# Performance work log

Measured on AMD Instinct MI355X. Metric: run time of the kernel, lower is better.

Reference implementation:

```python
import jax, jax.numpy as jnp
import numpy as np

D_MODEL = 256; H = 8; D_FF = 1024; BLOCKS = 2
NUM_ITEMS = 200000; NUM_USERS = 100000; T_DLT = 512
B = 256; INTER = 50; INTRA = 20; CAND = 2048
NEG_INF = -1e9

def layer_norm(x, g, b, eps=1e-6):
    m = x.mean(-1, keepdims=True)
    s = x.std(-1, keepdims=True, ddof=1)  # torch .std is unbiased
    return g * (x - m) / (s + eps) + b

def pos_encoding(L, d):
    pos = jnp.arange(L, dtype=jnp.float32)[:, None]
    div = jnp.exp(jnp.arange(0, d, 2, dtype=jnp.float32) * (-jnp.log(10000.0) / d))
    pe = jnp.zeros((L, d), dtype=jnp.float32)
    pe = pe.at[:, 0::2].set(jnp.sin(pos * div))
    pe = pe.at[:, 1::2].set(jnp.cos(pos * div))
    return pe

def setup_inputs() -> dict:
    key = jax.random.key(0)
    ks = jax.random.split(key, 20)
    d = D_MODEL
    w = lambda k, shape, s: jax.random.normal(k, shape, dtype=jnp.float32) * s
    s = 1.0 / np.sqrt(d)
    inp = {}
    inp["item_emb"] = w(ks[0], (NUM_ITEMS, d), 0.02)
    inp["user_emb"] = w(ks[1], (NUM_USERS, d), 0.02)
    inp["time_emb"] = w(ks[2], (T_DLT, d), 0.02)
    inp["Wq"] = w(ks[3], (d, d), s); inp["bq"] = jnp.zeros((d,), jnp.float32)
    inp["Wk"] = w(ks[4], (d, d), s); inp["bk"] = jnp.zeros((d,), jnp.float32)
    inp["Wv"] = w(ks[5], (d, d), s); inp["bv"] = jnp.zeros((d,), jnp.float32)
    inp["Wo"] = w(ks[6], (d, d), s); inp["bo"] = jnp.zeros((d,), jnp.float32)
    inp["ln1_g"] = jnp.ones((d,), jnp.float32); inp["ln1_b"] = jnp.zeros((d,), jnp.float32)
    inp["W1"] = w(ks[7], (d, D_FF), s); inp["b1"] = jnp.zeros((D_FF,), jnp.float32)
    inp["W2"] = w(ks[8], (D_FF, d), 1.0 / np.sqrt(D_FF)); inp["b2"] = jnp.zeros((d,), jnp.float32)
    inp["ln2_g"] = jnp.ones((d,), jnp.float32); inp["ln2_b"] = jnp.zeros((d,), jnp.float32)
    inp["fn_g"] = jnp.ones((d,), jnp.float32); inp["fn_b"] = jnp.zeros((d,), jnp.float32)
    inp["gate_Wl"] = w(ks[9], (d, d), s)
    inp["gate_Ws"] = w(ks[10], (d, d), s)
    inp["gate_Wt"] = w(ks[11], (d, d), s)
    inp["gate_bias"] = w(ks[12], (1, d), s)
    inp["batch_us"] = jax.random.randint(ks[13], (B,), 1, NUM_USERS)
    inp["batch_sessions"] = jax.random.randint(ks[14], (B, INTER, INTRA), 0, NUM_ITEMS)
    inp["batch_timedlt"] = jax.random.randint(ks[15], (B,), 0, T_DLT)
    inp["batch_to_predict"] = jax.random.randint(ks[16], (B, CAND), 1, NUM_ITEMS)
    return inp

def reference(item_emb, user_emb, time_emb, Wq, bq, Wk, bk, Wv, bv, Wo, bo,
              ln1_g, ln1_b, W1, b1, W2, b2, ln2_g, ln2_b, fn_g, fn_b,
              gate_Wl, gate_Ws, gate_Wt, gate_bias,
              batch_us, batch_sessions, batch_timedlt, batch_to_predict):
    d = D_MODEL
    item_e = item_emb.at[0].set(0.0)  # padding_idx=0
    user_e = user_emb.at[0].set(0.0)
    E = item_e[batch_sessions]              # [B, INTER, INTRA, d]
    U_embs = user_e[batch_us]               # [B, d]
    t_embs = time_emb[batch_timedlt]        # [B, d]
    Bsz = E.shape[0]
    # intra-session attention (single-head scaled dot-product, padding mask only)
    x = E.reshape(-1, INTRA, d)             # [B*INTER, INTRA, d]
    pad1 = (batch_sessions.reshape(-1, INTRA) != 0)[:, None, :]
    scores = jnp.einsum('nqd,nkd->nqk', x, x) / jnp.sqrt(jnp.float32(d))
    p = jax.nn.softmax(jnp.where(pad1, scores, NEG_INF), axis=-1)
    atted = jnp.einsum('nqk,nkd->nqd', p, x)
    E_hat = atted.sum(axis=1).reshape(Bsz, INTER, d)
    u_short = E_hat[:, -1, :]
    pad2 = (batch_sessions[:, :, 0] != 0)[:, None, None, :]   # [B,1,1,INTER]
    S = E_hat + pos_encoding(INTER, d)[None]
    dh = d // H
    for _ in range(BLOCKS):  # same sublayer applied blocks times (shared weights)
        y = layer_norm(S, ln1_g, ln1_b)
        q = (y @ Wq + bq).reshape(Bsz, INTER, H, dh)
        k = (y @ Wk + bk).reshape(Bsz, INTER, H, dh)
        v = (y @ Wv + bv).reshape(Bsz, INTER, H, dh)
        att = jnp.einsum('bqhe,bkhe->bhqk', q, k) / jnp.sqrt(jnp.float32(dh))
        aw = jax.nn.softmax(jnp.where(pad2, att, NEG_INF), axis=-1)
        o = jnp.einsum('bhqk,bkhe->bqhe', aw, v).reshape(Bsz, INTER, d)
        S = S + o @ Wo + bo
        y2 = layer_norm(S, ln2_g, ln2_b)
        S = S + jax.nn.relu(y2 @ W1 + b1) @ W2 + b2
    S1 = layer_norm(S, fn_g, fn_b)
    u_long = S1.sum(axis=1) + U_embs
    Tg = jax.nn.sigmoid(u_long @ gate_Wl + u_short @ gate_Ws + t_embs @ gate_Wt + gate_bias)
    U = Tg * u_short + (1.0 - Tg) * u_long
    cand = item_e[batch_to_predict]         # [B, CAND, d]
    return jnp.einsum('bcd,bd->bc', cand, U)
```

## Files before the change

### kernel.cpp

```cpp
#include <hip/hip_runtime.h>
#include <math.h>

#define D 256
#define HEADS 8
#define DH 32
#define INTER 50
#define INTRA 20
#define BSZ 256
#define CANDN 2048
#define ROWS (BSZ*INTER)
#define NITEMS 200000

typedef unsigned short ushort_t;
typedef __attribute__((ext_vector_type(8))) short bf16x8;
typedef __attribute__((ext_vector_type(4))) float f32x4;

__device__ __forceinline__ unsigned short f2b(float f) {
    union { float f; unsigned u; } v; v.f = f;
    unsigned r = v.u + 0x7fffu + ((v.u >> 16) & 1u);
    return (unsigned short)(r >> 16);
}
__device__ __forceinline__ float b2f(unsigned short h) {
    union { unsigned u; float f; } v; v.u = ((unsigned)h) << 16;
    return v.f;
}

__device__ __forceinline__ void wtr_body(const float* __restrict__ W, int K, int N,
    unsigned short* __restrict__ WT, int bx, int by, float (*tile)[33], int t)
{
    int n0 = bx*32, k0 = by*32;
    int tx = t & 31, ty = t >> 5;
    for (int i = ty; i < 32; i += 8)
        tile[i][tx] = W[(size_t)(k0+i)*N + n0 + tx];
    __syncthreads();
    for (int i = ty; i < 32; i += 8)
        WT[(size_t)(n0+i)*K + k0 + tx] = f2b(tile[tx][i]);
}

__global__ __launch_bounds__(256) void prep_k(
    const float* __restrict__ item_emb, unsigned short* __restrict__ item_b, int itemBlocks,
    const float* __restrict__ Wq, const float* __restrict__ Wk,
    const float* __restrict__ Wv, const float* __restrict__ Wo,
    const float* __restrict__ W1, const float* __restrict__ W2,
    unsigned short* __restrict__ WqkvT, unsigned short* __restrict__ WoT,
    unsigned short* __restrict__ W1T, unsigned short* __restrict__ W2T,
    const float* __restrict__ bq, const float* __restrict__ bk,
    const float* __restrict__ bv, float* __restrict__ bqkv)
{
    __shared__ float tile[32][33];
    int blk = blockIdx.x, t = threadIdx.x;
    if (blk < itemBlocks) {
        int i = blk*256 + t;
        float4 v = ((const float4*)item_emb)[i];
        ushort4 h; h.x=f2b(v.x); h.y=f2b(v.y); h.z=f2b(v.z); h.w=f2b(v.w);
        ((ushort4*)item_b)[i] = h;
        return;
    }
    blk -= itemBlocks;
    if (blk < 64)       wtr_body(Wq, 256, 256,  WqkvT,            blk & 7,  blk >> 3, tile, t);
    else if (blk < 128) wtr_body(Wk, 256, 256,  WqkvT + 256*256, (blk-64) & 7,  (blk-64) >> 3, tile, t);
    else if (blk < 192) wtr_body(Wv, 256, 256,  WqkvT + 512*256, (blk-128) & 7, (blk-128) >> 3, tile, t);
    else if (blk < 256) wtr_body(Wo, 256, 256,  WoT,             (blk-192) & 7, (blk-192) >> 3, tile, t);
    else if (blk < 512) { int id = blk-256; wtr_body(W1, 256, 1024, W1T, id & 31, id >> 5, tile, t); }
    else if (blk < 768) { int id = blk-512; wtr_body(W2, 1024, 256, W2T, id & 7,  id >> 3, tile, t); }
    else { bqkv[t] = bq[t]; bqkv[256+t] = bk[t]; bqkv[512+t] = bv[t]; }
}

#define XST 264
__global__ __launch_bounds__(256) void intra_k(
    const float* __restrict__ item_emb, const unsigned short* __restrict__ item_b,
    const int* __restrict__ sess,
    float* __restrict__ S, float* __restrict__ u_short)
{
    __shared__ __align__(16) unsigned short xb[4][INTRA][XST];
    __shared__ __align__(16) unsigned short zrow[XST];
    __shared__ float sc[4][20][21];
    __shared__ float wsum[4][20];
    __shared__ int ids[4][INTRA];
    int t = threadIdx.x, w = t >> 6, lane = t & 63;
    int s = blockIdx.x*4 + w;
    if (lane < INTRA) ids[w][lane] = sess[s*INTRA + lane];
    if (t < 132) ((unsigned int*)zrow)[t] = 0u;
    __syncthreads();
    int col = lane*4;
    for (int r = 0; r < INTRA; ++r) {
        int id = ids[w][r];
        ushort4 h;
        if (id == 0) { h.x=h.y=h.z=h.w=0; }
        else if (item_b) {
            h = *(const ushort4*)(item_b + (size_t)id*D + col);
        } else {
            float4 v4 = *(const float4*)(item_emb + (size_t)id*D + col);
            h.x=f2b(v4.x); h.y=f2b(v4.y); h.z=f2b(v4.z); h.w=f2b(v4.w);
        }
        *(ushort4*)&xb[w][r][col] = h;
    }
    __syncthreads();
    int ml = lane & 15, q8 = (lane >> 4) * 8;
    int r1 = 16 + ml;
    f32x4 acc[2][2] = {};
    for (int k0 = 0; k0 < D; k0 += 32) {
        bf16x8 fr0 = *(const bf16x8*)&xb[w][ml][k0 + q8];
        bf16x8 fr1 = (r1 < INTRA) ? *(const bf16x8*)&xb[w][r1][k0 + q8]
                                  : *(const bf16x8*)&zrow[q8];
        acc[0][0] = __builtin_amdgcn_mfma_f32_16x16x32_bf16(fr0, fr0, acc[0][0], 0,0,0);
        acc[0][1] = __builtin_amdgcn_mfma_f32_16x16x32_bf16(fr0, fr1, acc[0][1], 0,0,0);
        acc[1][0] = __builtin_amdgcn_mfma_f32_16x16x32_bf16(fr1, fr0, acc[1][0], 0,0,0);
        acc[1][1] = __builtin_amdgcn_mfma_f32_16x16x32_bf16(fr1, fr1, acc[1][1], 0,0,0);
    }
    int rb = (lane >> 4) * 4;
    #pragma unroll
    for (int mt = 0; mt < 2; ++mt)
        #pragma unroll
        for (int nt = 0; nt < 2; ++nt)
            #pragma unroll
            for (int i = 0; i < 4; ++i) {
                int row = mt*16 + rb + i, cc = nt*16 + ml;
                if (row < INTRA && cc < INTRA) sc[w][row][cc] = acc[mt][nt][i];
            }
    __syncthreads();
    if (lane < INTRA) {
        float vrow[INTRA]; float mx = -1e30f;
        #pragma unroll
        for (int k = 0; k < INTRA; ++k) {
            float v_ = (ids[w][k] != 0) ? sc[w][lane][k]*(1.0f/16.0f) : -1e9f;
            vrow[k] = v_; mx = fmaxf(mx, v_);
        }
        float ssum = 0.f;
        #pragma unroll
        for (int k = 0; k < INTRA; ++k) { float e_ = expf(vrow[k]-mx); vrow[k]=e_; ssum+=e_; }
        float inv = 1.f/ssum;
        #pragma unroll
        for (int k = 0; k < INTRA; ++k) sc[w][lane][k] = vrow[k]*inv;
    }
    __syncthreads();
    if (lane < INTRA) {
        float s_ = 0.f;
        #pragma unroll
        for (int q = 0; q < INTRA; ++q) s_ += sc[w][q][lane];
        wsum[w][lane] = s_;
    }
    __syncthreads();
    float4 v = {0.f,0.f,0.f,0.f};
    #pragma unroll
    for (int k = 0; k < INTRA; ++k) {
        float ws_ = wsum[w][k];
        ushort4 h = *(const ushort4*)&xb[w][k][col];
        v.x += ws_*b2f(h.x); v.y += ws_*b2f(h.y);
        v.z += ws_*b2f(h.z); v.w += ws_*b2f(h.w);
    }
    int b = s / INTER, srow = s % INTER;
    if (srow == INTER-1) *(float4*)(u_short + (size_t)b*D + col) = v;
    const float kc = -9.210340371976184f / 256.0f;
    float div0 = expf((float)col * kc);
    float div2 = expf((float)(col+2) * kc);
    float4 o;
    o.x = v.x + sinf((float)srow * div0);
    o.y = v.y + cosf((float)srow * div0);
    o.z = v.z + sinf((float)srow * div2);
    o.w = v.w + cosf((float)srow * div2);
    *(float4*)(S + (size_t)s*D + col) = o;
}

#define LB_VT 0
#define LB_Y 36864
#define LB_Q 70656
#define LB_K 104448
#define LB_PB 36864
#define LB_O 110592
#define LB_SL 0
#define LB_Y2 52000
#define LB_H 85792
#define LB_MSK 152352
#define MFMA16(a,b,c) __builtin_amdgcn_mfma_f32_16x16x32_bf16(a, b, c, 0, 0, 0)

__global__ __launch_bounds__(512) void block_k(
    float* __restrict__ S,
    const unsigned short* __restrict__ WqkvT, const float* __restrict__ bqkv,
    const unsigned short* __restrict__ WoT, const float* __restrict__ bo,
    const unsigned short* __restrict__ W1T, const float* __restrict__ b1,
    const unsigned short* __restrict__ W2T, const float* __restrict__ b2,
    const float* __restrict__ ln1_g, const float* __restrict__ ln1_b,
    const float* __restrict__ ln2_g, const float* __restrict__ ln2_b,
    const int* __restrict__ sess)
{
    __shared__ __align__(16) char LB[152608];
    unsigned short* Yp  = (unsigned short*)(LB + LB_Y);
    unsigned short* Qp  = (unsigned short*)(LB + LB_Q);
    unsigned short* Kp  = (unsigned short*)(LB + LB_K);
    unsigned short* VTp = (unsigned short*)(LB + LB_VT);
    unsigned short* Op  = (unsigned short*)(LB + LB_O);
    unsigned short* Y2p = (unsigned short*)(LB + LB_Y2);
    unsigned short* Hp  = (unsigned short*)(LB + LB_H);
    float* Slp  = (float*)(LB + LB_SL);
    float* mskp = (float*)(LB + LB_MSK);

    int b = blockIdx.x;
    int t = threadIdx.x, w = t >> 6, lane = t & 63;
    int ml = lane & 15, q8 = (lane >> 4) * 8;
    int col_l = ml, rbase = (lane >> 4) * 4;
    float* Sg = S + (size_t)b * INTER * D;

    if (t < 64) mskp[t] = (t < 50 && sess[(b*INTER + t)*INTRA] != 0) ? 1.f : 0.f;
    for (int u = t; u < 14*256; u += 512) {
        int r = 50 + (u >> 8), c = u & 255;
        Yp[r*264 + c] = 0; Qp[r*264 + c] = 0; Kp[r*264 + c] = 0;
    }
    for (int u = t; u < 8*32*14; u += 512) {
        int hh = u / 448, rem = u % 448;
        VTp[(hh*32 + rem/14)*72 + 50 + rem%14] = 0;
    }
    {
        int col = lane*4;
        float4 g4 = *(const float4*)(ln1_g + col), b4 = *(const float4*)(ln1_b + col);
        for (int r = w; r < 50; r += 8) {
            float4 x = *(const float4*)(Sg + r*256 + col);
            float s_ = x.x + x.y + x.z + x.w;
            #pragma unroll
            for (int o = 32; o > 0; o >>= 1) s_ += __shfl_xor(s_, o, 64);
            float mean = s_ * (1.f/256.f);
            float dx = x.x-mean, dy = x.y-mean, dz = x.z-mean, dw = x.w-mean;
            float qq = dx*dx + dy*dy + dz*dz + dw*dw;
            #pragma unroll
            for (int o = 32; o > 0; o >>= 1) qq += __shfl_xor(qq, o, 64);
            float inv = 1.f/(sqrtf(qq*(1.f/255.f)) + 1e-6f);
            ushort4 h;
            h.x = f2b(g4.x*dx*inv + b4.x); h.y = f2b(g4.y*dy*inv + b4.y);
            h.z = f2b(g4.z*dz*inv + b4.z); h.w = f2b(g4.w*dw*inv + b4.w);
            *(ushort4*)&Yp[r*264 + col] = h;
        }
    }
    __syncthreads();

    {
        f32x4 acc[4][6] = {};
        #pragma unroll
        for (int ks = 0; ks < 8; ++ks) {
            bf16x8 af[4];
            #pragma unroll
            for (int mt = 0; mt < 4; ++mt)
                af[mt] = *(const bf16x8*)&Yp[(mt*16+ml)*264 + ks*32 + q8];
            bf16x8 bfr[6];
            #pragma unroll
            for (int j = 0; j < 6; ++j) {
                int n = (w*6 + j)*16 + ml;
                bfr[j] = *(const bf16x8*)(WqkvT + (size_t)n*256 + ks*32 + q8);
            }
            #pragma unroll
            for (int j = 0; j < 6; ++j)
                #pragma unroll
                for (int mt = 0; mt < 4; ++mt)
                    acc[mt][j] = MFMA16(af[mt], bfr[j], acc[mt][j]);
        }
        #pragma unroll
        for (int j = 0; j < 6; ++j) {
            int n = (w*6 + j)*16 + col_l;
            float bs = bqkv[n];
            #pragma unroll
            for (int mt = 0; mt < 4; ++mt)
                #pragma unroll
                for (int i = 0; i < 4; ++i) {
                    int row = mt*16 + rbase + i;
                    if (row < 50) {
                        unsigned short hv = f2b(acc[mt][j][i] + bs);
                        if (n < 256)      Qp[row*264 + n] = hv;
                        else if (n < 512) Kp[row*264 + (n-256)] = hv;
                        else { int hh=(n-512)>>5, e=(n-512)&31; VTp[(hh*32+e)*72 + row] = hv; }
                    }
                }
        }
    }
    __syncthreads();

    unsigned short* pbw = (unsigned short*)(LB + LB_PB + w*9216);
    {
        f32x4 p3[4][4] = {};
        {
            bf16x8 af[4], bf_[4];
            #pragma unroll
            for (int mt = 0; mt < 4; ++mt)
                af[mt] = *(const bf16x8*)&Qp[(mt*16+ml)*264 + w*32 + q8];
            #pragma unroll
            for (int nt = 0; nt < 4; ++nt)
                bf_[nt] = *(const bf16x8*)&Kp[(nt*16+ml)*264 + w*32 + q8];
            #pragma unroll
            for (int mt = 0; mt < 4; ++mt)
                #pragma unroll
                for (int nt = 0; nt < 4; ++nt)
                    p3[mt][nt] = MFMA16(af[mt], bf_[nt], p3[mt][nt]);
        }
        float mk[4];
        #pragma unroll
        for (int nt = 0; nt < 4; ++nt) mk[nt] = mskp[nt*16 + ml];
        __syncthreads();
        #pragma unroll
        for (int mt = 0; mt < 4; ++mt)
            #pragma unroll
            for (int i = 0; i < 4; ++i) {
                int row = mt*16 + rbase + i;
                float v[4]; float m = -1e30f;
                #pragma unroll
                for (int nt = 0; nt < 4; ++nt) {
                    float x = (mk[nt] != 0.f) ? p3[mt][nt][i]*0.17677669529663687f : -1e9f;
                    v[nt] = x; m = fmaxf(m, x);
                }
                #pragma unroll
                for (int o = 8; o > 0; o >>= 1) m = fmaxf(m, __shfl_xor(m, o, 64));
                float s_ = 0.f;
                #pragma unroll
                for (int nt = 0; nt < 4; ++nt) { v[nt] = expf(v[nt] - m); s_ += v[nt]; }
                #pragma unroll
                for (int o = 8; o > 0; o >>= 1) s_ += __shfl_xor(s_, o, 64);
                float inv = 1.f / s_;
                if (row < 50) {
                    #pragma unroll
                    for (int nt = 0; nt < 4; ++nt)
                        pbw[row*72 + nt*16 + ml] = f2b(v[nt]*inv);
                }
            }
    }
    {
        f32x4 po[4][2] = {};
        #pragma unroll
        for (int kt = 0; kt < 2; ++kt) {
            bf16x8 af[4], bv_[2];
            #pragma unroll
            for (int mt = 0; mt < 4; ++mt)
                af[mt] = *(const bf16x8*)&pbw[(mt*16+ml)*72 + kt*32 + q8];
            #pragma unroll
            for (int nt = 0; nt < 2; ++nt)
                bv_[nt] = *(const bf16x8*)&VTp[(w*32 + nt*16 + ml)*72 + kt*32 + q8];
            #pragma unroll
            for (int nt = 0; nt < 2; ++nt)
                #pragma unroll
                for (int mt = 0; mt < 4; ++mt)
                    po[mt][nt] = MFMA16(af[mt], bv_[nt], po[mt][nt]);
        }
        #pragma unroll
        for (int nt = 0; nt < 2; ++nt)
            #pragma unroll
            for (int mt = 0; mt < 4; ++mt)
                #pragma unroll
                for (int i = 0; i < 4; ++i) {
                    int row = mt*16 + rbase + i;
                    if (row < 50)
                        Op[row*264 + w*32 + nt*16 + col_l] = f2b(po[mt][nt][i]);
                }
    }
    __syncthreads();

    {
        f32x4 a5[4][2] = {};
        #pragma unroll
        for (int ks = 0; ks < 8; ++ks) {
            bf16x8 af[4], bw[2];
            #pragma unroll
            for (int mt = 0; mt < 4; ++mt)
                af[mt] = *(const bf16x8*)&Op[(mt*16+ml)*264 + ks*32 + q8];
            #pragma unroll
            for (int j = 0; j < 2; ++j) {
                int n = w*32 + j*16 + ml;
                bw[j] = *(const bf16x8*)(WoT + (size_t)n*256 + ks*32 + q8);
            }
            #pragma unroll
            for (int j = 0; j < 2; ++j)
                #pragma unroll
                for (int mt = 0; mt < 4; ++mt)
                    a5[mt][j] = MFMA16(af[mt], bw[j], a5[mt][j]);
        }
        #pragma unroll
        for (int j = 0; j < 2; ++j) {
            int n = w*32 + j*16 + col_l;
            float bv = bo[n];
            #pragma unroll
            for (int mt = 0; mt < 4; ++mt)
                #pragma unroll
                for (int i = 0; i < 4; ++i) {
                    int row = mt*16 + rbase + i;
                    if (row < 50)
                        Slp[row*260 + n] = Sg[row*256 + n] + a5[mt][j][i] + bv;
                }
        }
    }
    __syncthreads();

    {
        int col = lane*4;
        float4 g4 = *(const float4*)(ln2_g + col), b4 = *(const float4*)(ln2_b + col);
        for (int r = w; r < 50; r += 8) {
            float4 x = *(const float4*)&Slp[r*260 + col];
            float s_ = x.x + x.y + x.z + x.w;
            #pragma unroll
            for (int o = 32; o > 0; o >>= 1) s_ += __shfl_xor(s_, o, 64);
            float mean = s_ * (1.f/256.f);
            float dx = x.x-mean, dy = x.y-mean, dz = x.z-mean, dw = x.w-mean;
            float qq = dx*dx + dy*dy + dz*dz + dw*dw;
            #pragma unroll
            for (int o = 32; o > 0; o >>= 1) qq += __shfl_xor(qq, o, 64);
            float inv = 1.f/(sqrtf(qq*(1.f/255.f)) + 1e-6f);
            ushort4 h;
            h.x = f2b(g4.x*dx*inv + b4.x); h.y = f2b(g4.y*dy*inv + b4.y);
            h.z = f2b(g4.z*dz*inv + b4.z); h.w = f2b(g4.w*dw*inv + b4.w);
            *(ushort4*)&Y2p[r*264 + col] = h;
        }
        for (int u = t; u < 14*256; u += 512) {
            int r = 50 + (u >> 8), c = u & 255;
            Y2p[r*264 + c] = 0;
        }
    }
    __syncthreads();

    #pragma unroll
    for (int hf = 0; hf < 2; ++hf) {
        {
            f32x4 a7[4][4] = {};
            #pragma unroll
            for (int ks = 0; ks < 8; ++ks) {
                bf16x8 af[4], bw[4];
                #pragma unroll
                for (int mt = 0; mt < 4; ++mt)
                    af[mt] = *(const bf16x8*)&Y2p[(mt*16+ml)*264 + ks*32 + q8];
                #pragma unroll
                for (int j = 0; j < 4; ++j) {
                    int n = hf*512 + w*64 + j*16 + ml;
                    bw[j] = *(const bf16x8*)(W1T + (size_t)n*256 + ks*32 + q8);
                }
                #pragma unroll
                for (int j = 0; j < 4; ++j)
                    #pragma unroll
                    for (int mt = 0; mt < 4; ++mt)
                        a7[mt][j] = MFMA16(af[mt], bw[j], a7[mt][j]);
            }
            #pragma unroll
            for (int j = 0; j < 4; ++j) {
                int nl = w*64 + j*16 + col_l;
                float bv = b1[hf*512 + nl];
                #pragma unroll
                for (int mt = 0; mt < 4; ++mt)
                    #pragma unroll
                    for (int i = 0; i < 4; ++i) {
                        int row = mt*16 + rbase + i;
                        if (row < 50)
                            Hp[row*520 + nl] = f2b(fmaxf(a7[mt][j][i] + bv, 0.f));
                    }
            }
        }
        __syncthreads();
        {
            f32x4 a8[4][2] = {};
            #pragma unroll
            for (int ks = 0; ks < 16; ++ks) {
                bf16x8 af[4], bw[2];
                #pragma unroll
                for (int mt = 0; mt < 4; ++mt)
                    af[mt] = *(const bf16x8*)&Hp[(mt*16+ml)*520 + ks*32 + q8];
                #pragma unroll
                for (int j = 0; j < 2; ++j) {
                    int n = w*32 + j*16 + ml;
                    bw[j] = *(const bf16x8*)(W2T + (size_t)n*1024 + hf*512 + ks*32 + q8);
                }
                #pragma unroll
                for (int j = 0; j < 2; ++j)
                    #pragma unroll
                    for (int mt = 0; mt < 4; ++mt)
                        a8[mt][j] = MFMA16(af[mt], bw[j], a8[mt][j]);
            }
            #pragma unroll
            for (int j = 0; j < 2; ++j) {
                int n = w*32 + j*16 + col_l;
                float bv = (hf == 0) ? b2[n] : 0.f;
                #pragma unroll
                for (int mt = 0; mt < 4; ++mt)
                    #pragma unroll
                    for (int i = 0; i < 4; ++i) {
                        int row = mt*16 + rbase + i;
                        if (row < 50)
                            Slp[row*260 + n] += a8[mt][j][i] + bv;
                    }
            }
        }
        __syncthreads();
    }

    for (int u = t; u < 50*256; u += 512) {
        int r = u >> 8, c = u & 255;
        Sg[r*256 + c] = Slp[r*260 + c];
    }
}

__global__ __launch_bounds__(256) void tail_k(
    const float* __restrict__ S,
    const float* __restrict__ fn_g, const float* __restrict__ fn_b,
    const float* __restrict__ user_emb, const int* __restrict__ us,
    const float* __restrict__ time_emb, const int* __restrict__ tdlt,
    const float* __restrict__ u_short,
    const float* __restrict__ Wl, const float* __restrict__ Ws,
    const float* __restrict__ Wt, const float* __restrict__ gb,
    float* __restrict__ U)
{
    __shared__ float part[4][D];
    __shared__ float ul[D], ush[D], te[D];
    int b = blockIdx.x, t = threadIdx.x, w = t >> 6, lane = t & 63;
    int col = lane*4;
    float4 g4 = *(const float4*)(fn_g + col);
    float4 b4 = *(const float4*)(fn_b + col);
    float4 acc4 = {0.f,0.f,0.f,0.f};
    for (int l = w; l < INTER; l += 4) {
        float4 x = *(const float4*)(S + (size_t)(b*INTER + l)*D + col);
        float s = x.x + x.y + x.z + x.w;
        #pragma unroll
        for (int o = 32; o > 0; o >>= 1) s += __shfl_xor(s, o, 64);
        float mean = s * (1.f/256.f);
        float dx = x.x - mean, dy = x.y - mean, dz = x.z - mean, dw = x.w - mean;
        float q = dx*dx + dy*dy + dz*dz + dw*dw;
        #pragma unroll
        for (int o = 32; o > 0; o >>= 1) q += __shfl_xor(q, o, 64);
        float inv = 1.f/(sqrtf(q*(1.f/255.f)) + 1e-6f);
        acc4.x += g4.x*dx*inv + b4.x;
        acc4.y += g4.y*dy*inv + b4.y;
        acc4.z += g4.z*dz*inv + b4.z;
        acc4.w += g4.w*dw*inv + b4.w;
    }
    *(float4*)&part[w][col] = acc4;
    __syncthreads();
    int id = us[b];
    float ue = (id == 0) ? 0.f : user_emb[(size_t)id*D + t];
    float ulv = part[0][t] + part[1][t] + part[2][t] + part[3][t] + ue;
    ul[t]  = ulv;
    float ushv = u_short[b*D + t];
    ush[t] = ushv;
    te[t]  = time_emb[(size_t)tdlt[b]*D + t];
    __syncthreads();
    float a = gb[t];
    for (int k = 0; k < D; ++k)
        a += ul[k]*Wl[k*D + t] + ush[k]*Ws[k*D + t] + te[k]*Wt[k*D + t];
    float tg = 1.f/(1.f + expf(-a));
    U[b*D + t] = tg*ushv + (1.f - tg)*ulv;
}

__global__ __launch_bounds__(256) void out_k(
    const float* __restrict__ item_emb, const unsigned short* __restrict__ item_b,
    const int* __restrict__ pred,
    const float* __restrict__ U, float* __restrict__ out)
{
    int b = blockIdx.x >> 6;
    int cbase = (blockIdx.x & 63) * 32;
    int t = threadIdx.x, w = t >> 6, lane = t & 63;
    int hl = lane & 31, half = lane >> 5;
    float4 u0 = *(const float4*)(U + (size_t)b*D + hl*8);
    float4 u1 = *(const float4*)(U + (size_t)b*D + hl*8 + 4);
    for (int it = 0; it < 4; ++it) {
        int c = cbase + it*8 + w*2 + half;
        int id = pred[b*CANDN + c];
        float p = 0.f;
        if (id) {
            if (item_b) {
                const unsigned short* row = item_b + (size_t)id*D + hl*8;
                ushort4 a = *(const ushort4*)row;
                ushort4 d = *(const ushort4*)(row+4);
                p = b2f(a.x)*u0.x + b2f(a.y)*u0.y + b2f(a.z)*u0.z + b2f(a.w)*u0.w
                  + b2f(d.x)*u1.x + b2f(d.y)*u1.y + b2f(d.z)*u1.z + b2f(d.w)*u1.w;
            } else {
                const float* row = item_emb + (size_t)id*D + hl*8;
                float4 a = *(const float4*)row;
                float4 d = *(const float4*)(row+4);
                p = a.x*u0.x + a.y*u0.y + a.z*u0.z + a.w*u0.w
                  + d.x*u1.x + d.y*u1.y + d.z*u1.z + d.w*u1.w;
            }
        }
        #pragma unroll
        for (int off = 16; off > 0; off >>= 1) p += __shfl_xor(p, off, 64);
        if (hl == 0) out[b*CANDN + c] = p;
    }
}

extern "C" void kernel_launch(void* const* d_in, const int* in_sizes, int n_in,
                              void* d_out, int out_size, void* d_ws, size_t ws_size,
                              hipStream_t stream)
{
    const float* item_emb = (const float*)d_in[0];
    const float* user_emb = (const float*)d_in[1];
    const float* time_emb = (const float*)d_in[2];
    const float* Wq = (const float*)d_in[3];  const float* bq = (const float*)d_in[4];
    const float* Wk = (const float*)d_in[5];  const float* bk = (const float*)d_in[6];
    const float* Wv = (const float*)d_in[7];  const float* bv = (const float*)d_in[8];
    const float* Wo = (const float*)d_in[9];  const float* bo = (const float*)d_in[10];
    const float* ln1_g = (const float*)d_in[11]; const float* ln1_b = (const float*)d_in[12];
    const float* W1 = (const float*)d_in[13]; const float* b1 = (const float*)d_in[14];
    const float* W2 = (const float*)d_in[15]; const float* b2 = (const float*)d_in[16];
    const float* ln2_g = (const float*)d_in[17]; const float* ln2_b = (const float*)d_in[18];
    const float* fn_g = (const float*)d_in[19]; const float* fn_b = (const float*)d_in[20];
    const float* gWl = (const float*)d_in[21]; const float* gWs = (const float*)d_in[22];
    const float* gWt = (const float*)d_in[23]; const float* gbias = (const float*)d_in[24];
    const int* us   = (const int*)d_in[25];
    const int* sess = (const int*)d_in[26];
    const int* tdlt = (const int*)d_in[27];
    const int* pred = (const int*)d_in[28];
    float* out = (float*)d_out;

    char* base = (char*)d_ws;
    size_t off = 0;
    float* S = (float*)(base+off);              off += (size_t)ROWS*D*4;
    unsigned short* WqkvT = (unsigned short*)(base+off); off += (size_t)768*256*2;
    unsigned short* WoT   = (unsigned short*)(base+off); off += (size_t)256*256*2;
    unsigned short* W1T   = (unsigned short*)(base+off); off += (size_t)1024*256*2;
    unsigned short* W2T   = (unsigned short*)(base+off); off += (size_t)256*1024*2;
    float* bqkv = (float*)(base+off);            off += 768*4;
    float* u_short = (float*)(base+off);         off += BSZ*D*4;
    float* Ufin    = (float*)(base+off);         off += BSZ*D*4;
    unsigned short* item_b = (unsigned short*)(base+off);
    size_t item_b_bytes = (size_t)NITEMS*D*2;
    bool use_b16 = (off + item_b_bytes) <= ws_size;
    if (!use_b16) item_b = nullptr;

    int itemBlocks = use_b16 ? (NITEMS*D/4)/256 : 0;
    prep_k<<<itemBlocks + 769, 256, 0, stream>>>(
        item_emb, item_b, itemBlocks,
        Wq, Wk, Wv, Wo, W1, W2,
        WqkvT, WoT, W1T, W2T,
        bq, bk, bv, bqkv);

    intra_k<<<ROWS/4, 256, 0, stream>>>(item_emb, item_b, sess, S, u_short);

    for (int blk = 0; blk < 2; ++blk)
        block_k<<<BSZ, 512, 0, stream>>>(S, WqkvT, bqkv, WoT, bo,
                                         W1T, b1, W2T, b2,
                                         ln1_g, ln1_b, ln2_g, ln2_b, sess);

    tail_k<<<BSZ, 256, 0, stream>>>(S, fn_g, fn_b, user_emb, us,
        time_emb, tdlt, u_short, gWl, gWs, gWt, gbias, Ufin);

    out_k<<<(BSZ*CANDN)/32, 256, 0, stream>>>(item_emb, item_b, pred, Ufin, out);
}
```

Baseline: 677.4 us.

## Fuse both transformer blocks and final norm into one 1024-thread kernel

Both shared-weight transformer blocks now run inside a single block_k launch that loops twice, so the second launch and part of the global reload of S go away. The final layer norm and the sum over the sequence move into the same kernel, which writes a per-batch u_long vector that tail_k reads. The workgroup grows from 512 to 1024 threads, and each wave takes half the earlier GEMM and attention work, meaning two waves per head. Zeroing of the padded Y, Q, K and Y2 rows is dropped; the code relies on masking and on discarding rows at or beyond 50 to keep results correct.

```diff
diff --git a/kernel.cpp b/kernel.cpp
--- a/kernel.cpp
+++ b/kernel.cpp
@@ -174,7 +174,7 @@
 #define LB_MSK 152352
 #define MFMA16(a,b,c) __builtin_amdgcn_mfma_f32_16x16x32_bf16(a, b, c, 0, 0, 0)
 
-__global__ __launch_bounds__(512) void block_k(
+__global__ __launch_bounds__(1024) void block_k(
     float* __restrict__ S,
     const unsigned short* __restrict__ WqkvT, const float* __restrict__ bqkv,
     const unsigned short* __restrict__ WoT, const float* __restrict__ bo,
@@ -182,7 +182,8 @@
     const unsigned short* __restrict__ W2T, const float* __restrict__ b2,
     const float* __restrict__ ln1_g, const float* __restrict__ ln1_b,
     const float* __restrict__ ln2_g, const float* __restrict__ ln2_b,
-    const int* __restrict__ sess)
+    const float* __restrict__ fn_g, const float* __restrict__ fn_b,
+    const int* __restrict__ sess, float* __restrict__ u_long_raw)
 {
     __shared__ __align__(16) char LB[152608];
     unsigned short* Yp  = (unsigned short*)(LB + LB_Y);
@@ -199,22 +200,282 @@
     int t = threadIdx.x, w = t >> 6, lane = t & 63;
     int ml = lane & 15, q8 = (lane >> 4) * 8;
     int col_l = ml, rbase = (lane >> 4) * 4;
+    int h = w >> 1, half = w & 1;
     float* Sg = S + (size_t)b * INTER * D;
 
     if (t < 64) mskp[t] = (t < 50 && sess[(b*INTER + t)*INTRA] != 0) ? 1.f : 0.f;
-    for (int u = t; u < 14*256; u += 512) {
-        int r = 50 + (u >> 8), c = u & 255;
-        Yp[r*264 + c] = 0; Qp[r*264 + c] = 0; Kp[r*264 + c] = 0;
-    }
-    for (int u = t; u < 8*32*14; u += 512) {
-        int hh = u / 448, rem = u % 448;
-        VTp[(hh*32 + rem/14)*72 + 50 + rem%14] = 0;
-    }
+
+    for (int blk = 0; blk < 2; ++blk) {
+        for (int u = t; u < 8*32*14; u += 1024) {
+            int hh = u / 448, rem = u % 448;
+            VTp[(hh*32 + rem/14)*72 + 50 + rem%14] = 0;
+        }
+        {
+            int col = lane*4;
+            float4 g4 = *(const float4*)(ln1_g + col), b4 = *(const float4*)(ln1_b + col);
+            for (int r = w; r < 50; r += 16) {
+                float4 x = *(const float4*)(Sg + r*256 + col);
+                float s_ = x.x + x.y + x.z + x.w;
+                #pragma unroll
+                for (int o = 32; o > 0; o >>= 1) s_ += __shfl_xor(s_, o, 64);
+                float mean = s_ * (1.f/256.f);
+                float dx = x.x-mean, dy = x.y-mean, dz = x.z-mean, dw = x.w-mean;
+                float qq = dx*dx + dy*dy + dz*dz + dw*dw;
+                #pragma unroll
+                for (int o = 32; o > 0; o >>= 1) qq += __shfl_xor(qq, o, 64);
+                float inv = 1.f/(sqrtf(qq*(1.f/255.f)) + 1e-6f);
+                ushort4 hh4;
+                hh4.x = f2b(g4.x*dx*inv + b4.x); hh4.y = f2b(g4.y*dy*inv + b4.y);
+                hh4.z = f2b(g4.z*dz*inv + b4.z); hh4.w = f2b(g4.w*dw*inv + b4.w);
+                *(ushort4*)&Yp[r*264 + col] = hh4;
+            }
+        }
+        __syncthreads();
+
+        {
+            f32x4 acc[4][3] = {};
+            #pragma unroll
+            for (int ks = 0; ks < 8; ++ks) {
+                bf16x8 af[4];
+                #pragma unroll
+                for (int mt = 0; mt < 4; ++mt)
+                    af[mt] = *(const bf16x8*)&Yp[(mt*16+ml)*264 + ks*32 + q8];
+                bf16x8 bfr[3];
+                #pragma unroll
+                for (int j = 0; j < 3; ++j) {
+                    int n = (w*3 + j)*16 + ml;
+                    bfr[j] = *(const bf16x8*)(WqkvT + (size_t)n*256 + ks*32 + q8);
+                }
+                #pragma unroll
+                for (int j = 0; j < 3; ++j)
+                    #pragma unroll
+                    for (int mt = 0; mt < 4; ++mt)
+                        acc[mt][j] = MFMA16(af[mt], bfr[j], acc[mt][j]);
+            }
+            #pragma unroll
+            for (int j = 0; j < 3; ++j) {
+                int n = (w*3 + j)*16 + col_l;
+                float bs = bqkv[n];
+                #pragma unroll
+                for (int mt = 0; mt < 4; ++mt)
+                    #pragma unroll
+                    for (int i = 0; i < 4; ++i) {
+                        int row = mt*16 + rbase + i;
+                        if (row < 50) {
+                            unsigned short hv = f2b(acc[mt][j][i] + bs);
+                            if (n < 256)      Qp[row*264 + n] = hv;
+                            else if (n < 512) Kp[row*264 + (n-256)] = hv;
+                            else { int hh=(n-512)>>5, e=(n-512)&31; VTp[(hh*32+e)*72 + row] = hv; }
+                        }
+                    }
+            }
+        }
+        __syncthreads();
+
+        unsigned short* pbw = (unsigned short*)(LB + LB_PB + h*9216);
+        {
+            f32x4 p3[2][4] = {};
+            {
+                bf16x8 af[2], bf_[4];
+                #pragma unroll
+                for (int mt2 = 0; mt2 < 2; ++mt2)
+                    af[mt2] = *(const bf16x8*)&Qp[((half*2+mt2)*16+ml)*264 + h*32 + q8];
+                #pragma unroll
+                for (int nt = 0; nt < 4; ++nt)
+                    bf_[nt] = *(const bf16x8*)&Kp[(nt*16+ml)*264 + h*32 + q8];
+                #pragma unroll
+                for (int mt2 = 0; mt2 < 2; ++mt2)
+                    #pragma unroll
+                    for (int nt = 0; nt < 4; ++nt)
+                        p3[mt2][nt] = MFMA16(af[mt2], bf_[nt], p3[mt2][nt]);
+            }
+            float mk[4];
+            #pragma unroll
+            for (int nt = 0; nt < 4; ++nt) mk[nt] = mskp[nt*16 + ml];
+            __syncthreads();
+            #pragma unroll
+            for (int mt2 = 0; mt2 < 2; ++mt2)
+                #pragma unroll
+                for (int i = 0; i < 4; ++i) {
+                    int row = (half*2+mt2)*16 + rbase + i;
+                    float v[4]; float m = -1e30f;
+                    #pragma unroll
+                    for (int nt = 0; nt < 4; ++nt) {
+                        float x = (mk[nt] != 0.f) ? p3[mt2][nt][i]*0.17677669529663687f : -1e9f;
+                        v[nt] = x; m = fmaxf(m, x);
+                    }
+                    #pragma unroll
+                    for (int o = 8; o > 0; o >>= 1) m = fmaxf(m, __shfl_xor(m, o, 64));
+                    float s_ = 0.f;
+                    #pragma unroll
+                    for (int nt = 0; nt < 4; ++nt) { v[nt] = expf(v[nt] - m); s_ += v[nt]; }
+                    #pragma unroll
+                    for (int o = 8; o > 0; o >>= 1) s_ += __shfl_xor(s_, o, 64);
+                    float inv = 1.f / s_;
+                    if (row < 50) {
+                        #pragma unroll
+                        for (int nt = 0; nt < 4; ++nt)
+                            pbw[row*72 + nt*16 + ml] = f2b(v[nt]*inv);
+                    }
+                }
+        }
+        {
+            f32x4 po[2][2] = {};
+            #pragma unroll
+            for (int kt = 0; kt < 2; ++kt) {
+                bf16x8 af[2], bv_[2];
+                #pragma unroll
+                for (int mt2 = 0; mt2 < 2; ++mt2)
+                    af[mt2] = *(const bf16x8*)&pbw[((half*2+mt2)*16+ml)*72 + kt*32 + q8];
+                #pragma unroll
+                for (int nt = 0; nt < 2; ++nt)
+                    bv_[nt] = *(const bf16x8*)&VTp[(h*32 + nt*16 + ml)*72 + kt*32 + q8];
+                #pragma unroll
+                for (int nt = 0; nt < 2; ++nt)
+                    #pragma unroll
+                    for (int mt2 = 0; mt2 < 2; ++mt2)
+                        po[mt2][nt] = MFMA16(af[mt2], bv_[nt], po[mt2][nt]);
+            }
+            #pragma unroll
+            for (int nt = 0; nt < 2; ++nt)
+                #pragma unroll
+                for (int mt2 = 0; mt2 < 2; ++mt2)
+                    #pragma unroll
+                    for (int i = 0; i < 4; ++i) {
+                        int row = (half*2+mt2)*16 + rbase + i;
+                        if (row < 50)
+                            Op[row*264 + h*32 + nt*16 + col_l] = f2b(po[mt2][nt][i]);
+                    }
+        }
+        __syncthreads();
+
+        {
+            f32x4 a5[4] = {};
+            #pragma unroll
+            for (int ks = 0; ks < 8; ++ks) {
+                bf16x8 af[4], bw;
+                #pragma unroll
+                for (int mt = 0; mt < 4; ++mt)
+                    af[mt] = *(const bf16x8*)&Op[(mt*16+ml)*264 + ks*32 + q8];
+                bw = *(const bf16x8*)(WoT + (size_t)(w*16+ml)*256 + ks*32 + q8);
+                #pragma unroll
+                for (int mt = 0; mt < 4; ++mt)
+                    a5[mt] = MFMA16(af[mt], bw, a5[mt]);
+            }
+            int n = w*16 + col_l;
+            float bv = bo[n];
+            #pragma unroll
+            for (int mt = 0; mt < 4; ++mt)
+                #pragma unroll
+                for (int i = 0; i < 4; ++i) {
+                    int row = mt*16 + rbase + i;
+                    if (row < 50)
+                        Slp[row*260 + n] = Sg[row*256 + n] + a5[mt][i] + bv;
+                }
+        }
+        __syncthreads();
+
+        {
+            int col = lane*4;
+            float4 g4 = *(const float4*)(ln2_g + col), b4 = *(const float4*)(ln2_b + col);
+            for (int r = w; r < 50; r += 16) {
+                float4 x = *(const float4*)&Slp[r*260 + col];
+                float s_ = x.x + x.y + x.z + x.w;
+                #pragma unroll
+                for (int o = 32; o > 0; o >>= 1) s_ += __shfl_xor(s_, o, 64);
+                float mean = s_ * (1.f/256.f);
+                float dx = x.x-mean, dy = x.y-mean, dz = x.z-mean, dw = x.w-mean;
+                float qq = dx*dx + dy*dy + dz*dz + dw*dw;
+                #pragma unroll
+                for (int o = 32; o > 0; o >>= 1) qq += __shfl_xor(qq, o, 64);
+                float inv = 1.f/(sqrtf(qq*(1.f/255.f)) + 1e-6f);
+                ushort4 hh4;
+                hh4.x = f2b(g4.x*dx*inv + b4.x); hh4.y = f2b(g4.y*dy*inv + b4.y);
+                hh4.z = f2b(g4.z*dz*inv + b4.z); hh4.w = f2b(g4.w*dw*inv + b4.w);
+                *(ushort4*)&Y2p[r*264 + col] = hh4;
+            }
+        }
+        __syncthreads();
+
+        #pragma unroll
+        for (int hf = 0; hf < 2; ++hf) {
+            {
+                f32x4 a7[4][2] = {};
+                #pragma unroll
+                for (int ks = 0; ks < 8; ++ks) {
+                    bf16x8 af[4], bw[2];
+                    #pragma unroll
+                    for (int mt = 0; mt < 4; ++mt)
+                        af[mt] = *(const bf16x8*)&Y2p[(mt*16+ml)*264 + ks*32 + q8];
+                    #pragma unroll
+                    for (int j = 0; j < 2; ++j) {
+                        int n = hf*512 + (w*2+j)*16 + ml;
+                        bw[j] = *(const bf16x8*)(W1T + (size_t)n*256 + ks*32 + q8);
+                    }
+                    #pragma unroll
+                    for (int j = 0; j < 2; ++j)
+                        #pragma unroll
+                        for (int mt = 0; mt < 4; ++mt)
+                            a7[mt][j] = MFMA16(af[mt], bw[j], a7[mt][j]);
+                }
+                #pragma unroll
+                for (int j = 0; j < 2; ++j) {
+                    int nl = (w*2+j)*16 + col_l;
+                    float bv = b1[hf*512 + nl];
+                    #pragma unroll
+                    for (int mt = 0; mt < 4; ++mt)
+                        #pragma unroll
+                        for (int i = 0; i < 4; ++i) {
+                            int row = mt*16 + rbase + i;
+                            if (row < 50)
+                                Hp[row*520 + nl] = f2b(fmaxf(a7[mt][j][i] + bv, 0.f));
+                        }
+                }
+            }
+            __syncthreads();
+            {
+                f32x4 a8[4] = {};
+                #pragma unroll
+                for (int ks = 0; ks < 16; ++ks) {
+                    bf16x8 af[4], bw;
+                    #pragma unroll
+                    for (int mt = 0; mt < 4; ++mt)
+                        af[mt] = *(const bf16x8*)&Hp[(mt*16+ml)*520 + ks*32 + q8];
+                    bw = *(const bf16x8*)(W2T + (size_t)(w*16+ml)*1024 + hf*512 + ks*32 + q8);
+                    #pragma unroll
+                    for (int mt = 0; mt < 4; ++mt)
+                        a8[mt] = MFMA16(af[mt], bw, a8[mt]);
+                }
+                int n = w*16 + col_l;
+                float bv = (hf == 0) ? b2[n] : 0.f;
+                #pragma unroll
+                for (int mt = 0; mt < 4; ++mt)
+                    #pragma unroll
+                    for (int i = 0; i < 4; ++i) {
+                        int row = mt*16 + rbase + i;
+                        if (row < 50)
+                            Slp[row*260 + n] += a8[mt][i] + bv;
+                    }
+            }
+            __syncthreads();
+        }
+
+        if (blk == 0) {
+            for (int u = t; u < 50*256; u += 1024) {
+                int r = u >> 8, c = u & 255;
+                Sg[r*256 + c] = Slp[r*260 + c];
+            }
+            __syncthreads();
+        }
+    }
+
     {
+        float* partp = (float*)(LB + LB_H);
         int col = lane*4;
-        float4 g4 = *(const float4*)(ln1_g + col), b4 = *(const float4*)(ln1_b + col);
-        for (int r = w; r < 50; r += 8) {
-            float4 x = *(const float4*)(Sg + r*256 + col);
+        float4 g4 = *(const float4*)(fn_g + col), b4 = *(const float4*)(fn_b + col);
+        float4 acc4 = {0.f,0.f,0.f,0.f};
+        for (int r = w; r < 50; r += 16) {
+            float4 x = *(const float4*)&Slp[r*260 + col];
             float s_ = x.x + x.y + x.z + x.w;
             #pragma unroll
             for (int o = 32; o > 0; o >>= 1) s_ += __shfl_xor(s_, o, 64);
@@ -224,273 +485,24 @@
             #pragma unroll
             for (int o = 32; o > 0; o >>= 1) qq += __shfl_xor(qq, o, 64);
             float inv = 1.f/(sqrtf(qq*(1.f/255.f)) + 1e-6f);
-            ushort4 h;
-            h.x = f2b(g4.x*dx*inv + b4.x); h.y = f2b(g4.y*dy*inv + b4.y);
-            h.z = f2b(g4.z*dz*inv + b4.z); h.w = f2b(g4.w*dw*inv + b4.w);
-            *(ushort4*)&Yp[r*264 + col] = h;
-        }
-    }
-    __syncthreads();
-
-    {
-        f32x4 acc[4][6] = {};
-        #pragma unroll
-        for (int ks = 0; ks < 8; ++ks) {
-            bf16x8 af[4];
-            #pragma unroll
-            for (int mt = 0; mt < 4; ++mt)
-                af[mt] = *(const bf16x8*)&Yp[(mt*16+ml)*264 + ks*32 + q8];
-            bf16x8 bfr[6];
-            #pragma unroll
-            for (int j = 0; j < 6; ++j) {
-                int n = (w*6 + j)*16 + ml;
-                bfr[j] = *(const bf16x8*)(WqkvT + (size_t)n*256 + ks*32 + q8);
-            }
-            #pragma unroll
-            for (int j = 0; j < 6; ++j)
-                #pragma unroll
-                for (int mt = 0; mt < 4; ++mt)
-                    acc[mt][j] = MFMA16(af[mt], bfr[j], acc[mt][j]);
-        }
-        #pragma unroll
-        for (int j = 0; j < 6; ++j) {
-            int n = (w*6 + j)*16 + col_l;
-            float bs = bqkv[n];
-            #pragma unroll
-            for (int mt = 0; mt < 4; ++mt)
-                #pragma unroll
-                for (int i = 0; i < 4; ++i) {
-                    int row = mt*16 + rbase + i;
-                    if (row < 50) {
-                        unsigned short hv = f2b(acc[mt][j][i] + bs);
-                        if (n < 256)      Qp[row*264 + n] = hv;
-                        else if (n < 512) Kp[row*264 + (n-256)] = hv;
-                        else { int hh=(n-512)>>5, e=(n-512)&31; VTp[(hh*32+e)*72 + row] = hv; }
-                    }
-                }
-        }
-    }
-    __syncthreads();
-
-    unsigned short* pbw = (unsigned short*)(LB + LB_PB + w*9216);
-    {
-        f32x4 p3[4][4] = {};
-        {
-            bf16x8 af[4], bf_[4];
-            #pragma unroll
-            for (int mt = 0; mt < 4; ++mt)
-                af[mt] = *(const bf16x8*)&Qp[(mt*16+ml)*264 + w*32 + q8];
-            #pragma unroll
-            for (int nt = 0; nt < 4; ++nt)
-                bf_[nt] = *(const bf16x8*)&Kp[(nt*16+ml)*264 + w*32 + q8];
-            #pragma unroll
-            for (int mt = 0; mt < 4; ++mt)
-                #pragma unroll
-                for (int nt = 0; nt < 4; ++nt)
-                    p3[mt][nt] = MFMA16(af[mt], bf_[nt], p3[mt][nt]);
-        }
-        float mk[4];
-        #pragma unroll
-        for (int nt = 0; nt < 4; ++nt) mk[nt] = mskp[nt*16 + ml];
+            acc4.x += g4.x*dx*inv + b4.x;
+            acc4.y += g4.y*dy*inv + b4.y;
+            acc4.z += g4.z*dz*inv + b4.z;
+            acc4.w += g4.w*dw*inv + b4.w;
+        }
+        *(float4*)&partp[w*256 + col] = acc4;
         __syncthreads();
-        #pragma unroll
-        for (int mt = 0; mt < 4; ++mt)
-            #pragma unroll
-            for (int i = 0; i < 4; ++i) {
-                int row = mt*16 + rbase + i;
-                float v[4]; float m = -1e30f;
-                #pragma unroll
-                for (int nt = 0; nt < 4; ++nt) {
-                    float x = (mk[nt] != 0.f) ? p3[mt][nt][i]*0.17677669529663687f : -1e9f;
-                    v[nt] = x; m = fmaxf(m, x);
-                }
-                #pragma unroll
-                for (int o = 8; o > 0; o >>= 1) m = fmaxf(m, __shfl_xor(m, o, 64));
-                float s_ = 0.f;
-                #pragma unroll
-                for (int nt = 0; nt < 4; ++nt) { v[nt] = expf(v[nt] - m); s_ += v[nt]; }
-                #pragma unroll
-                for (int o = 8; o > 0; o >>= 1) s_ += __shfl_xor(s_, o, 64);
-                float inv = 1.f / s_;
-                if (row < 50) {
-                    #pragma unroll
-                    for (int nt = 0; nt < 4; ++nt)
-                        pbw[row*72 + nt*16 + ml] = f2b(v[nt]*inv);
-                }
-            }
-    }
-    {
-        f32x4 po[4][2] = {};
-        #pragma unroll
-        for (int kt = 0; kt < 2; ++kt) {
-            bf16x8 af[4], bv_[2];
-            #pragma unroll
-            for (int mt = 0; mt < 4; ++mt)
-                af[mt] = *(const bf16x8*)&pbw[(mt*16+ml)*72 + kt*32 + q8];
-            #pragma unroll
-            for (int nt = 0; nt < 2; ++nt)
-                bv_[nt] = *(const bf16x8*)&VTp[(w*32 + nt*16 + ml)*72 + kt*32 + q8];
-            #pragma unroll
-            for (int nt = 0; nt < 2; ++nt)
-                #pragma unroll
-                for (int mt = 0; mt < 4; ++mt)
-                    po[mt][nt] = MFMA16(af[mt], bv_[nt], po[mt][nt]);
-        }
-        #pragma unroll
-        for (int nt = 0; nt < 2; ++nt)
-            #pragma unroll
-            for (int mt = 0; mt < 4; ++mt)
-                #pragma unroll
-                for (int i = 0; i < 4; ++i) {
-                    int row = mt*16 + rbase + i;
-                    if (row < 50)
-                        Op[row*264 + w*32 + nt*16 + col_l] = f2b(po[mt][nt][i]);
-                }
-    }
-    __syncthreads();
-
-    {
-        f32x4 a5[4][2] = {};
-        #pragma unroll
-        for (int ks = 0; ks < 8; ++ks) {
-            bf16x8 af[4], bw[2];
-            #pragma unroll
-            for (int mt = 0; mt < 4; ++mt)
-                af[mt] = *(const bf16x8*)&Op[(mt*16+ml)*264 + ks*32 + q8];
-            #pragma unroll
-            for (int j = 0; j < 2; ++j) {
-                int n = w*32 + j*16 + ml;
-                bw[j] = *(const bf16x8*)(WoT + (size_t)n*256 + ks*32 + q8);
-            }
-            #pragma unroll
-            for (int j = 0; j < 2; ++j)
-                #pragma unroll
-                for (int mt = 0; mt < 4; ++mt)
-                    a5[mt][j] = MFMA16(af[mt], bw[j], a5[mt][j]);
-        }
-        #pragma unroll
-        for (int j = 0; j < 2; ++j) {
-            int n = w*32 + j*16 + col_l;
-            float bv = bo[n];
-            #pragma unroll
-            for (int mt = 0; mt < 4; ++mt)
-                #pragma unroll
-                for (int i = 0; i < 4; ++i) {
-                    int row = mt*16 + rbase + i;
-                    if (row < 50)
-                        Slp[row*260 + n] = Sg[row*256 + n] + a5[mt][j][i] + bv;
-                }
-        }
-    }
-    __syncthreads();
-
-    {
-        int col = lane*4;
-        float4 g4 = *(const float4*)(ln2_g + col), b4 = *(const float4*)(ln2_b + col);
-        for (int r = w; r < 50; r += 8) {
-            float4 x = *(const float4*)&Slp[r*260 + col];
-            float s_ = x.x + x.y + x.z + x.w;
-            #pragma unroll
-            for (int o = 32; o > 0; o >>= 1) s_ += __shfl_xor(s_, o, 64);
-            float mean = s_ * (1.f/256.f);
-            float dx = x.x-mean, dy = x.y-mean, dz = x.z-mean, dw = x.w-mean;
-            float qq = dx*dx + dy*dy + dz*dz + dw*dw;
-            #pragma unroll
-            for (int o = 32; o > 0; o >>= 1) qq += __shfl_xor(qq, o, 64);
-            float inv = 1.f/(sqrtf(qq*(1.f/255.f)) + 1e-6f);
-            ushort4 h;
-            h.x = f2b(g4.x*dx*inv + b4.x); h.y = f2b(g4.y*dy*inv + b4.y);
-            h.z = f2b(g4.z*dz*inv + b4.z); h.w = f2b(g4.w*dw*inv + b4.w);
-            *(ushort4*)&Y2p[r*264 + col] = h;
-        }
-        for (int u = t; u < 14*256; u += 512) {
-            int r = 50 + (u >> 8), c = u & 255;
-            Y2p[r*264 + c] = 0;
-        }
-    }
-    __syncthreads();
-
-    #pragma unroll
-    for (int hf = 0; hf < 2; ++hf) {
-        {
-            f32x4 a7[4][4] = {};
-            #pragma unroll
-            for (int ks = 0; ks < 8; ++ks) {
-                bf16x8 af[4], bw[4];
-                #pragma unroll
-                for (int mt = 0; mt < 4; ++mt)
-                    af[mt] = *(const bf16x8*)&Y2p[(mt*16+ml)*264 + ks*32 + q8];
-                #pragma unroll
-                for (int j = 0; j < 4; ++j) {
-                    int n = hf*512 + w*64 + j*16 + ml;
-                    bw[j] = *(const bf16x8*)(W1T + (size_t)n*256 + ks*32 + q8);
-                }
-                #pragma unroll
-                for (int j = 0; j < 4; ++j)
-                    #pragma unroll
-                    for (int mt = 0; mt < 4; ++mt)
-                        a7[mt][j] = MFMA16(af[mt], bw[j], a7[mt][j]);
-            }
-            #pragma unroll
-            for (int j = 0; j < 4; ++j) {
-                int nl = w*64 + j*16 + col_l;
-                float bv = b1[hf*512 + nl];
-                #pragma unroll
-                for (int mt = 0; mt < 4; ++mt)
-                    #pragma unroll
-                    for (int i = 0; i < 4; ++i) {
-                        int row = mt*16 + rbase + i;
-                        if (row < 50)
-                            Hp[row*520 + nl] = f2b(fmaxf(a7[mt][j][i] + bv, 0.f));
-                    }
-            }
-        }
-        __syncthreads();
-        {
-            f32x4 a8[4][2] = {};
-            #pragma unroll
-            for (int ks = 0; ks < 16; ++ks) {
-                bf16x8 af[4], bw[2];
-                #pragma unroll
-                for (int mt = 0; mt < 4; ++mt)
-                    af[mt] = *(const bf16x8*)&Hp[(mt*16+ml)*520 + ks*32 + q8];
-                #pragma unroll
-                for (int j = 0; j < 2; ++j) {
-                    int n = w*32 + j*16 + ml;
-                    bw[j] = *(const bf16x8*)(W2T + (size_t)n*1024 + hf*512 + ks*32 + q8);
-                }
-                #pragma unroll
-                for (int j = 0; j < 2; ++j)
-                    #pragma unroll
-                    for (int mt = 0; mt < 4; ++mt)
-                        a8[mt][j] = MFMA16(af[mt], bw[j], a8[mt][j]);
-            }
-            #pragma unroll
-            for (int j = 0; j < 2; ++j) {
-                int n = w*32 + j*16 + col_l;
-                float bv = (hf == 0) ? b2[n] : 0.f;
-                #pragma unroll
-                for (int mt = 0; mt < 4; ++mt)
-                    #pragma unroll
-                    for (int i = 0; i < 4; ++i) {
-                        int row = mt*16 + rbase + i;
-                        if (row < 50)
-                            Slp[row*260 + n] += a8[mt][j][i] + bv;
-                    }
-            }
-        }
-        __syncthreads();
-    }
-
-    for (int u = t; u < 50*256; u += 512) {
-        int r = u >> 8, c = u & 255;
-        Sg[r*256 + c] = Slp[r*260 + c];
+        if (t < 256) {
+            float s_ = 0.f;
+            #pragma unroll
+            for (int ww = 0; ww < 16; ++ww) s_ += partp[ww*256 + t];
+            u_long_raw[(size_t)b*D + t] = s_;
+        }
     }
 }
 
 __global__ __launch_bounds__(256) void tail_k(
-    const float* __restrict__ S,
-    const float* __restrict__ fn_g, const float* __restrict__ fn_b,
+    const float* __restrict__ u_long_raw,
     const float* __restrict__ user_emb, const int* __restrict__ us,
     const float* __restrict__ time_emb, const int* __restrict__ tdlt,
     const float* __restrict__ u_short,
@@ -498,34 +510,11 @@
     const float* __restrict__ Wt, const float* __restrict__ gb,
     float* __restrict__ U)
 {
-    __shared__ float part[4][D];
     __shared__ float ul[D], ush[D], te[D];
-    int b = blockIdx.x, t = threadIdx.x, w = t >> 6, lane = t & 63;
-    int col = lane*4;
-    float4 g4 = *(const float4*)(fn_g + col);
-    float4 b4 = *(const float4*)(fn_b + col);
-    float4 acc4 = {0.f,0.f,0.f,0.f};
-    for (int l = w; l < INTER; l += 4) {
-        float4 x = *(const float4*)(S + (size_t)(b*INTER + l)*D + col);
-        float s = x.x + x.y + x.z + x.w;
-        #pragma unroll
-        for (int o = 32; o > 0; o >>= 1) s += __shfl_xor(s, o, 64);
-        float mean = s * (1.f/256.f);
-        float dx = x.x - mean, dy = x.y - mean, dz = x.z - mean, dw = x.w - mean;
-        float q = dx*dx + dy*dy + dz*dz + dw*dw;
-        #pragma unroll
-        for (int o = 32; o > 0; o >>= 1) q += __shfl_xor(q, o, 64);
-        float inv = 1.f/(sqrtf(q*(1.f/255.f)) + 1e-6f);
-        acc4.x += g4.x*dx*inv + b4.x;
-        acc4.y += g4.y*dy*inv + b4.y;
-        acc4.z += g4.z*dz*inv + b4.z;
-        acc4.w += g4.w*dw*inv + b4.w;
-    }
-    *(float4*)&part[w][col] = acc4;
-    __syncthreads();
+    int b = blockIdx.x, t = threadIdx.x;
     int id = us[b];
     float ue = (id == 0) ? 0.f : user_emb[(size_t)id*D + t];
-    float ulv = part[0][t] + part[1][t] + part[2][t] + part[3][t] + ue;
+    float ulv = u_long_raw[(size_t)b*D + t] + ue;
     ul[t]  = ulv;
     float ushv = u_short[b*D + t];
     ush[t] = ushv;
@@ -607,6 +596,7 @@
     unsigned short* W2T   = (unsigned short*)(base+off); off += (size_t)256*1024*2;
     float* bqkv = (float*)(base+off);            off += 768*4;
     float* u_short = (float*)(base+off);         off += BSZ*D*4;
+    float* u_long  = (float*)(base+off);         off += BSZ*D*4;
     float* Ufin    = (float*)(base+off);         off += BSZ*D*4;
     unsigned short* item_b = (unsigned short*)(base+off);
     size_t item_b_bytes = (size_t)NITEMS*D*2;
@@ -622,12 +612,12 @@
 
     intra_k<<<ROWS/4, 256, 0, stream>>>(item_emb, item_b, sess, S, u_short);
 
-    for (int blk = 0; blk < 2; ++blk)
-        block_k<<<BSZ, 512, 0, stream>>>(S, WqkvT, bqkv, WoT, bo,
-                                         W1T, b1, W2T, b2,
-                                         ln1_g, ln1_b, ln2_g, ln2_b, sess);
-
-    tail_k<<<BSZ, 256, 0, stream>>>(S, fn_g, fn_b, user_emb, us,
+    block_k<<<BSZ, 1024, 0, stream>>>(S, WqkvT, bqkv, WoT, bo,
+                                      W1T, b1, W2T, b2,
+                                      ln1_g, ln1_b, ln2_g, ln2_b,
+                                      fn_g, fn_b, sess, u_long);
+
+    tail_k<<<BSZ, 256, 0, stream>>>(u_long, user_emb, us,
         time_emb, tdlt, u_short, gWl, gWs, gWt, gbias, Ufin);
 
     out_k<<<(BSZ*CANDN)/32, 256, 0, stream>>>(item_emb, item_b, pred, Ufin, out);
```

After: 976.5 us. +44.2%, slower.
